# Kernel optimization log

Measured on AMD Instinct MI355X. Metric: run time of the kernel, lower is better.

Reference implementation:

```python
import jax, jax.numpy as jnp
import numpy as np

B, S, H = 4, 1024, 2048      # batch, seq_len, hidden_size
N, D = 16, 128               # num_attention_heads, attention_head_size (num_kv_heads == N)
W_SCALE = 0.02


def setup_inputs() -> dict:
    key = jax.random.key(0)
    ks = jax.random.split(key, 7)
    hidden_states = jax.random.normal(ks[0], (B, S, H), dtype=jnp.float32)
    # Per-head query projections (stacked over the head axis) + shared K/V projections.
    Wq = jax.random.normal(ks[1], (N, H, D), dtype=jnp.float32) * W_SCALE
    bq = jax.random.normal(ks[2], (N, D), dtype=jnp.float32) * W_SCALE
    Wk = jax.random.normal(ks[3], (H, D), dtype=jnp.float32) * W_SCALE
    bk = jax.random.normal(ks[4], (D,), dtype=jnp.float32) * W_SCALE
    Wv = jax.random.normal(ks[5], (H, D), dtype=jnp.float32) * W_SCALE
    bv = jax.random.normal(ks[6], (D,), dtype=jnp.float32) * W_SCALE
    return {"hidden_states": hidden_states, "Wq": Wq, "bq": bq,
            "Wk": Wk, "bk": bk, "Wv": Wv, "bv": bv}


def reference(hidden_states, Wq, bq, Wk, bk, Wv, bv):
    # Batched equivalent of the per-head Python loop:
    # q_i = Linear_i(h); k = key_layer(h); v = value_layer(h) (shared across heads,
    # repeat_interleave is a no-op since num_kv_heads == num_attention_heads).
    Q = jnp.einsum('bsh,nhd->bnsd', hidden_states, Wq) + bq[None, :, None, :]  # [B,N,S,D]
    K = hidden_states @ Wk + bk   # [B,S,D]
    V = hidden_states @ Wv + bv   # [B,S,D]
    # NOTE: source applies no 1/sqrt(D) scaling.
    scores = jnp.einsum('bnsd,btd->bnst', Q, K)          # [B,N,S,S]
    attn = jax.nn.softmax(scores, axis=-1)
    out = jnp.einsum('bnst,btd->bnsd', attn, V)          # [B,N,S,D]
    return out
```

## Files before the change

kernel.cpp:

```cpp
#include <hip/hip_runtime.h>
#include <hip/hip_bf16.h>

typedef unsigned short ushort_t;
typedef _Float16 half_t;
typedef __attribute__((ext_vector_type(8))) _Float16 h8;
typedef __attribute__((ext_vector_type(8))) short short8;
typedef __attribute__((ext_vector_type(4))) short short4_t;
typedef __attribute__((ext_vector_type(4))) float f32x4;
typedef __attribute__((ext_vector_type(4))) float f4;

#define NB 4
#define SS 1024
#define HH 2048
#define NH 16
#define DD 128
#define MM (NB*SS)
#define NTOT 2304
#define COL_K 2048
#define COL_V 2176
#define KVB 64
#define L2E 1.44269504089f

__device__ __forceinline__ ushort_t f2h(float x) {
    half_t h = (half_t)x;
    return *(ushort_t*)&h;
}
__device__ __forceinline__ f32x4 mfma16h(h8 a, h8 b, f32x4 c) {
    return __builtin_amdgcn_mfma_f32_16x16x32_f16(a, b, c, 0, 0, 0);
}
__device__ __forceinline__ void load_lds16(const ushort_t* g, ushort_t* l) {
    __builtin_amdgcn_global_load_lds(
        (const __attribute__((address_space(1))) unsigned int*)g,
        (__attribute__((address_space(3))) unsigned int*)l,
        16, 0, 0);
}

__global__ void k_cvt(const float* __restrict__ src, ushort_t* __restrict__ dst, int n) {
    int i = (blockIdx.x * blockDim.x + threadIdx.x) * 8;
    if (i + 7 < n) {
        f4 a = *(const f4*)(src + i);
        f4 b = *(const f4*)(src + i + 4);
        short8 o;
        #pragma unroll
        for (int j = 0; j < 4; ++j) { o[j] = (short)f2h(a[j]); o[4 + j] = (short)f2h(b[j]); }
        *(short8*)(dst + i) = o;
    }
}

__global__ __launch_bounds__(256) void k_tw(const float* __restrict__ W,
                                            ushort_t* __restrict__ T, int Dd) {
    __shared__ ushort_t t[64][74];
    const int n = blockIdx.z;
    const int h0 = blockIdx.x * 64, d0 = blockIdx.y * 64;
    const int r = threadIdx.x >> 2, cg = (threadIdx.x & 3) * 16;
    const float* src = W + ((size_t)n * HH + h0 + r) * Dd + d0 + cg;
    #pragma unroll
    for (int v = 0; v < 4; ++v) {
        f4 a = *(const f4*)(src + v * 4);
        #pragma unroll
        for (int j = 0; j < 4; ++j) t[r][cg + v * 4 + j] = f2h(a[j]);
    }
    __syncthreads();
    short8 o0, o1;
    #pragma unroll
    for (int j = 0; j < 8; ++j) { o0[j] = (short)t[cg + j][r]; o1[j] = (short)t[cg + 8 + j][r]; }
    ushort_t* dst = T + ((size_t)(n * Dd + d0 + r)) * HH + h0 + cg;
    *(short8*)dst = o0;
    *(short8*)(dst + 8) = o1;
}

__global__ __launch_bounds__(256) void k_gemm(
    const ushort_t* __restrict__ A, const ushort_t* __restrict__ B,
    const float* __restrict__ bq, const float* __restrict__ bk,
    const float* __restrict__ bvv, ushort_t* __restrict__ O,
    ushort_t* __restrict__ Vt) {

    constexpr int BK = 32;
    __shared__ ushort_t sA[128 * BK], sB[128 * BK];

    const int bid = blockIdx.x;
    const int swz = (bid & 7) * 72 + (bid >> 3);
    const int m0 = (swz & 31) * 128;
    const int n0 = (swz >> 5) * 128;

    const int tid = threadIdx.x;
    const int w = tid >> 6, l = tid & 63;
    const int wr = w >> 1, wc = w & 1;
    f32x4 acc[4][4] = {};

    for (int kt = 0; kt < HH / BK; ++kt) {
        const int k0 = kt * BK;
        #pragma unroll
        for (int c = 0; c < 2; ++c) {
            int chunk = c * 4 + w;
            int idx = chunk * 512 + l * 8;
            int row = idx >> 5, kc = idx & 31;
            load_lds16(A + (size_t)(m0 + row) * HH + k0 + kc, &sA[chunk * 512]);
            load_lds16(B + (size_t)(n0 + row) * HH + k0 + kc, &sB[chunk * 512]);
        }
        __syncthreads();

        h8 a[4], b[4];
        #pragma unroll
        for (int i = 0; i < 4; ++i) {
            int ra = wr * 64 + i * 16 + (l & 15);
            int rb = wc * 64 + i * 16 + (l & 15);
            a[i] = *(const h8*)&sA[ra * 32 + (l >> 4) * 8];
            b[i] = *(const h8*)&sB[rb * 32 + (l >> 4) * 8];
        }
        #pragma unroll
        for (int i = 0; i < 4; ++i)
            #pragma unroll
            for (int j = 0; j < 4; ++j)
                acc[i][j] = mfma16h(a[i], b[j], acc[i][j]);
        __syncthreads();
    }

    #pragma unroll
    for (int i = 0; i < 4; ++i) {
        int row = m0 + wr * 64 + i * 16 + ((l >> 4) << 2);
        #pragma unroll
        for (int j = 0; j < 4; ++j) {
            int col = n0 + wc * 64 + j * 16 + (l & 15);
            float bv = (col < COL_K) ? bq[col]
                     : (col < COL_V) ? bk[col - COL_K]
                                     : bvv[col - COL_V];
            if (col < COL_V) {
                #pragma unroll
                for (int r = 0; r < 4; ++r)
                    O[(size_t)(row + r) * NTOT + col] = f2h(acc[i][j][r] + bv);
            } else {
                short4_t o;
                #pragma unroll
                for (int r = 0; r < 4; ++r) o[r] = (short)f2h(acc[i][j][r] + bv);
                *(short4_t*)&Vt[(size_t)(col - COL_V) * MM + row] = o;
            }
        }
    }
}

__global__ __launch_bounds__(512, 4) void k_attn(
    const ushort_t* __restrict__ O, const ushort_t* __restrict__ Vt,
    float* __restrict__ Out) {

    __shared__ ushort_t sK[2][KVB * 128];
    __shared__ ushort_t sVt[2][128 * KVB];

    const int tid = threadIdx.x;
    const int w = tid >> 6, l = tid & 63;
    const int lg = l >> 4, li = l & 15;
    const int q0 = blockIdx.x * 128;
    const int n = blockIdx.y, b = blockIdx.z;

    h8 qv[4];
    {
        size_t base = ((size_t)(b * SS + q0 + w * 16 + li)) * NTOT + n * 128 + lg * 8;
        #pragma unroll
        for (int kk = 0; kk < 4; ++kk)
            qv[kk] = *(const h8*)&O[base + kk * 32];
    }

    f32x4 accO[8] = {};
    float m2 = -3.0e38f;
    float lsum = 0.f;

    auto stage = [&](int bi, int t0) {
        #pragma unroll
        for (int c = 0; c < 2; ++c) {
            int seg = c * 8 + w;
            int oe = seg * 512 + l * 8;
            int row = oe >> 7;
            int mk = (row & 3) | (((row >> 3) & 3) << 2);
            int ce = (oe & 127) ^ (mk << 3);
            size_t g = (size_t)(b * SS + t0 + row) * NTOT + COL_K + ce;
            load_lds16(O + g, &sK[bi][seg * 512]);
        }
        #pragma unroll
        for (int c = 0; c < 2; ++c) {
            int seg = c * 8 + w;
            int oe = seg * 512 + l * 8;
            int row = oe >> 6;
            int ce = (oe & 63) ^ ((row & 7) << 3);
            size_t g = (size_t)row * MM + b * SS + t0 + ce;
            load_lds16(Vt + g, &sVt[bi][seg * 512]);
        }
    };

    stage(0, 0);
    constexpr int NT = SS / KVB;

    for (int it = 0; it < NT; ++it) {
        const int cur = it & 1;
        const int t0 = it * KVB;
        __syncthreads();
        if (it + 1 < NT) stage(cur ^ 1, t0 + KVB);
        const ushort_t* sKc = sK[cur];
        const ushort_t* sVc = sVt[cur];

        f32x4 s[4] = {};
        __builtin_amdgcn_s_setprio(1);
        #pragma unroll
        for (int ts = 0; ts < 4; ++ts) {
            int trow = (ts & 1) * 32 + ((li >> 2) << 3) + ((ts >> 1) << 2) + (li & 3);
            int mk = (trow & 3) | (((trow >> 3) & 3) << 2);
            #pragma unroll
            for (int kk = 0; kk < 4; ++kk) {
                h8 kv = *(const h8*)&sKc[trow * 128 + ((kk * 32 + lg * 8) ^ (mk << 3))];
                s[ts] = mfma16h(kv, qv[kk], s[ts]);
            }
        }
        __builtin_amdgcn_s_setprio(0);

        float v = fmaxf(fmaxf(s[0][0], s[0][1]), fmaxf(s[0][2], s[0][3]));
        #pragma unroll
        for (int ts = 1; ts < 4; ++ts)
            v = fmaxf(v, fmaxf(fmaxf(s[ts][0], s[ts][1]), fmaxf(s[ts][2], s[ts][3])));
        v = fmaxf(v, __shfl_xor(v, 16));
        v = fmaxf(v, __shfl_xor(v, 32));
        float pm2 = v * L2E;

        if (!__all(pm2 <= m2 + 11.54f)) {
            float mn = fmaxf(m2, pm2);
            float scl = exp2f(m2 - mn);
            lsum *= scl;
            #pragma unroll
            for (int db = 0; db < 8; ++db)
                #pragma unroll
                for (int r = 0; r < 4; ++r) accO[db][r] *= scl;
            m2 = mn;
        }

        h8 pb[2];
        #pragma unroll
        for (int ts = 0; ts < 4; ++ts)
            #pragma unroll
            for (int r = 0; r < 4; ++r) {
                float p = exp2f(fmaf(s[ts][r], L2E, -m2));
                lsum += p;
                pb[ts & 1][((ts >> 1) << 2) + r] = (half_t)p;
            }

        __builtin_amdgcn_s_setprio(1);
        #pragma unroll
        for (int db = 0; db < 8; ++db) {
            int d = db * 16 + li;
            const ushort_t* vbase = &sVc[d * KVB];
            int sw = (d & 7) << 3;
            #pragma unroll
            for (int ks = 0; ks < 2; ++ks) {
                h8 va = *(const h8*)&vbase[(ks * 32 + lg * 8) ^ sw];
                accO[db] = mfma16h(va, pb[ks], accO[db]);
            }
        }
        __builtin_amdgcn_s_setprio(0);
    }

    lsum += __shfl_xor(lsum, 16);
    lsum += __shfl_xor(lsum, 32);
    float inv = 1.0f / lsum;
    int q = q0 + w * 16 + li;
    size_t base = (((size_t)b * NH + n) * SS + q) * DD;
    #pragma unroll
    for (int db = 0; db < 8; ++db) {
        f4 o;
        #pragma unroll
        for (int r = 0; r < 4; ++r) o[r] = accO[db][r] * inv;
        *(f4*)&Out[base + db * 16 + lg * 4] = o;
    }
}

#define OFF_HC    ((size_t)0)
#define OFF_BC    (OFF_HC + (size_t)MM*HH*2)
#define OFF_O     (OFF_BC + (size_t)NTOT*HH*2)
#define OFF_VT    (OFF_O + (size_t)MM*NTOT*2)

extern "C" void kernel_launch(void* const* d_in, const int* in_sizes, int n_in,
                              void* d_out, int out_size, void* d_ws, size_t ws_size,
                              hipStream_t stream) {
    const float* hs = (const float*)d_in[0];
    const float* Wq = (const float*)d_in[1];
    const float* bq = (const float*)d_in[2];
    const float* Wk = (const float*)d_in[3];
    const float* bk = (const float*)d_in[4];
    const float* Wv = (const float*)d_in[5];
    const float* bv = (const float*)d_in[6];
    float* out = (float*)d_out;
    char* ws = (char*)d_ws;

    ushort_t* hc   = (ushort_t*)(ws + OFF_HC);
    ushort_t* bcat = (ushort_t*)(ws + OFF_BC);
    ushort_t* Obuf = (ushort_t*)(ws + OFF_O);
    ushort_t* vt   = (ushort_t*)(ws + OFF_VT);

    k_cvt<<<(MM*HH)/(256*8), 256, 0, stream>>>(hs, hc, MM*HH);
    dim3 gwq(HH/64, DD/64, NH);
    k_tw<<<gwq, 256, 0, stream>>>(Wq, bcat, DD);
    dim3 gwk(HH/64, DD/64, 1);
    k_tw<<<gwk, 256, 0, stream>>>(Wk, bcat + (size_t)COL_K*HH, DD);
    k_tw<<<gwk, 256, 0, stream>>>(Wv, bcat + (size_t)COL_V*HH, DD);

    k_gemm<<<(MM/128)*(NTOT/128), 256, 0, stream>>>(hc, bcat, bq, bk, bv, Obuf, vt);

    dim3 ga(SS/128, NH, NB);
    k_attn<<<ga, 512, 0, stream>>>(Obuf, vt, out);
}
```

Baseline: 128.8 us.

## Double-buffer GEMM LDS with BK=64, XOR swizzle, and async prefetch

Restructures the projection GEMM's main loop to double-buffer LDS tiles with a K-step of 64. The next tile is prefetched via direct-to-LDS loads while the current one is consumed, with explicit vmcnt waits and barriers. LDS columns are XOR-swizzled by row to avoid bank conflicts, MFMA issue is wrapped in raised priority, and launch bounds request 2 blocks per CU. The aim is to hide global-load latency and halve barrier count, at the cost of more LDS per block and more dependence on hand-placed waitcnt correctness.

```diff
diff --git a/kernel.cpp b/kernel.cpp
--- a/kernel.cpp
+++ b/kernel.cpp
@@ -69,14 +69,13 @@
     *(short8*)(dst + 8) = o1;
 }
 
-__global__ __launch_bounds__(256) void k_gemm(
+__global__ __launch_bounds__(256, 2) void k_gemm(
     const ushort_t* __restrict__ A, const ushort_t* __restrict__ B,
     const float* __restrict__ bq, const float* __restrict__ bk,
     const float* __restrict__ bvv, ushort_t* __restrict__ O,
     ushort_t* __restrict__ Vt) {
 
-    constexpr int BK = 32;
-    __shared__ ushort_t sA[128 * BK], sB[128 * BK];
+    __shared__ __align__(16) ushort_t lds[2][16384];
 
     const int bid = blockIdx.x;
     const int swz = (bid & 7) * 72 + (bid >> 3);
@@ -85,43 +84,68 @@
 
     const int tid = threadIdx.x;
     const int w = tid >> 6, l = tid & 63;
+    const int lg = l >> 4, li = l & 15;
     const int wr = w >> 1, wc = w & 1;
     f32x4 acc[4][4] = {};
 
-    for (int kt = 0; kt < HH / BK; ++kt) {
-        const int k0 = kt * BK;
-        #pragma unroll
-        for (int c = 0; c < 2; ++c) {
-            int chunk = c * 4 + w;
-            int idx = chunk * 512 + l * 8;
-            int row = idx >> 5, kc = idx & 31;
-            load_lds16(A + (size_t)(m0 + row) * HH + k0 + kc, &sA[chunk * 512]);
-            load_lds16(B + (size_t)(n0 + row) * HH + k0 + kc, &sB[chunk * 512]);
-        }
-        __syncthreads();
-
-        h8 a[4], b[4];
-        #pragma unroll
-        for (int i = 0; i < 4; ++i) {
-            int ra = wr * 64 + i * 16 + (l & 15);
-            int rb = wc * 64 + i * 16 + (l & 15);
-            a[i] = *(const h8*)&sA[ra * 32 + (l >> 4) * 8];
-            b[i] = *(const h8*)&sB[rb * 32 + (l >> 4) * 8];
-        }
-        #pragma unroll
-        for (int i = 0; i < 4; ++i)
-            #pragma unroll
-            for (int j = 0; j < 4; ++j)
-                acc[i][j] = mfma16h(a[i], b[j], acc[i][j]);
-        __syncthreads();
+    auto stage = [&](int buf, int kt) {
+        const int k0 = kt * 64;
+        #pragma unroll
+        for (int c = 0; c < 4; ++c) {
+            int seg = c * 4 + w;
+            int oe = seg * 512 + l * 8;
+            int row = oe >> 6;
+            int ce = (oe & 63) ^ ((row & 7) << 3);
+            load_lds16(A + (size_t)(m0 + row) * HH + k0 + ce, &lds[buf][seg * 512]);
+            load_lds16(B + (size_t)(n0 + row) * HH + k0 + ce, &lds[buf][8192 + seg * 512]);
+        }
+    };
+
+    stage(0, 0);
+    constexpr int NK = HH / 64;
+
+    for (int kt = 0; kt < NK; ++kt) {
+        const int cur = kt & 1;
+        __builtin_amdgcn_s_barrier();
+        if (kt + 1 < NK) {
+            stage(cur ^ 1, kt + 1);
+            asm volatile("s_waitcnt vmcnt(8)" ::: "memory");
+        } else {
+            asm volatile("s_waitcnt vmcnt(0)" ::: "memory");
+        }
+        __builtin_amdgcn_sched_barrier(0);
+        __builtin_amdgcn_s_barrier();
+        __builtin_amdgcn_sched_barrier(0);
+
+        const ushort_t* sA = &lds[cur][0];
+        const ushort_t* sB = &lds[cur][8192];
+        h8 a[2][4], b[2][4];
+        #pragma unroll
+        for (int kk = 0; kk < 2; ++kk)
+            #pragma unroll
+            for (int i = 0; i < 4; ++i) {
+                int ra = wr * 64 + i * 16 + li;
+                int rb = wc * 64 + i * 16 + li;
+                a[kk][i] = *(const h8*)&sA[ra * 64 + ((kk * 32 + lg * 8) ^ ((ra & 7) << 3))];
+                b[kk][i] = *(const h8*)&sB[rb * 64 + ((kk * 32 + lg * 8) ^ ((rb & 7) << 3))];
+            }
+        __builtin_amdgcn_s_setprio(1);
+        #pragma unroll
+        for (int kk = 0; kk < 2; ++kk)
+            #pragma unroll
+            for (int i = 0; i < 4; ++i)
+                #pragma unroll
+                for (int j = 0; j < 4; ++j)
+                    acc[i][j] = mfma16h(a[kk][i], b[kk][j], acc[i][j]);
+        __builtin_amdgcn_s_setprio(0);
     }
 
     #pragma unroll
     for (int i = 0; i < 4; ++i) {
-        int row = m0 + wr * 64 + i * 16 + ((l >> 4) << 2);
+        int row = m0 + wr * 64 + i * 16 + (lg << 2);
         #pragma unroll
         for (int j = 0; j < 4; ++j) {
-            int col = n0 + wc * 64 + j * 16 + (l & 15);
+            int col = n0 + wc * 64 + j * 16 + li;
             float bv = (col < COL_K) ? bq[col]
                      : (col < COL_V) ? bk[col - COL_K]
                                      : bvv[col - COL_V];
```

New measurement: 134.6 us. 4.5% more time.

## Switch attention kernel to 32x32x16 MFMA with 32 query rows per wave

Applied to the files above, without the earlier changes.

Rewrites the attention kernel to use 32x32x16 f16 MFMA instead of 16x16x32, giving each wave 32 query rows and halving the block to 256 threads (4 waves, 128 queries per block). The P matrix is repacked in registers using v_permlane32_swap instead of being reshaped through the old layout. The goal is fewer LDS reads per FLOP and fewer MFMA issues. In exchange each thread holds more accumulator registers, and occupancy drops because of the new launch bounds.

```diff
diff --git a/kernel.cpp b/kernel.cpp
--- a/kernel.cpp
+++ b/kernel.cpp
@@ -7,6 +7,7 @@
 typedef __attribute__((ext_vector_type(8))) short short8;
 typedef __attribute__((ext_vector_type(4))) short short4_t;
 typedef __attribute__((ext_vector_type(4))) float f32x4;
+typedef __attribute__((ext_vector_type(16))) float f32x16;
 typedef __attribute__((ext_vector_type(4))) float f4;
 
 #define NB 4
@@ -27,6 +28,9 @@
 }
 __device__ __forceinline__ f32x4 mfma16h(h8 a, h8 b, f32x4 c) {
     return __builtin_amdgcn_mfma_f32_16x16x32_f16(a, b, c, 0, 0, 0);
+}
+__device__ __forceinline__ f32x16 mfma32h(h8 a, h8 b, f32x16 c) {
+    return __builtin_amdgcn_mfma_f32_32x32x16_f16(a, b, c, 0, 0, 0);
 }
 __device__ __forceinline__ void load_lds16(const ushort_t* g, ushort_t* l) {
     __builtin_amdgcn_global_load_lds(
@@ -139,7 +143,7 @@
     }
 }
 
-__global__ __launch_bounds__(512, 4) void k_attn(
+__global__ __launch_bounds__(256, 2) void k_attn(
     const ushort_t* __restrict__ O, const ushort_t* __restrict__ Vt,
     float* __restrict__ Out) {
 
@@ -148,26 +152,29 @@
 
     const int tid = threadIdx.x;
     const int w = tid >> 6, l = tid & 63;
-    const int lg = l >> 4, li = l & 15;
+    const int li = l & 31, hi = l >> 5;
     const int q0 = blockIdx.x * 128;
     const int n = blockIdx.y, b = blockIdx.z;
-
-    h8 qv[4];
+    const int q = q0 + w * 32 + li;
+
+    const int mkK = (li & 3) | (((li >> 3) & 3) << 2);
+    const int mkV = li & 7;
+
+    h8 qv[8];
     {
-        size_t base = ((size_t)(b * SS + q0 + w * 16 + li)) * NTOT + n * 128 + lg * 8;
-        #pragma unroll
-        for (int kk = 0; kk < 4; ++kk)
-            qv[kk] = *(const h8*)&O[base + kk * 32];
-    }
-
-    f32x4 accO[8] = {};
-    float m2 = -3.0e38f;
-    float lsum = 0.f;
+        size_t base = ((size_t)(b * SS + q)) * NTOT + n * 128 + hi * 8;
+        #pragma unroll
+        for (int c = 0; c < 8; ++c)
+            qv[c] = *(const h8*)&O[base + c * 16];
+    }
+
+    f32x16 acc0 = {}, acc1 = {}, acc2 = {}, acc3 = {};
+    float m2 = -3.0e38f, lsum = 0.f;
 
     auto stage = [&](int bi, int t0) {
         #pragma unroll
-        for (int c = 0; c < 2; ++c) {
-            int seg = c * 8 + w;
+        for (int c = 0; c < 4; ++c) {
+            int seg = c * 4 + w;
             int oe = seg * 512 + l * 8;
             int row = oe >> 7;
             int mk = (row & 3) | (((row >> 3) & 3) << 2);
@@ -176,8 +183,8 @@
             load_lds16(O + g, &sK[bi][seg * 512]);
         }
         #pragma unroll
-        for (int c = 0; c < 2; ++c) {
-            int seg = c * 8 + w;
+        for (int c = 0; c < 4; ++c) {
+            int seg = c * 4 + w;
             int oe = seg * 512 + l * 8;
             int row = oe >> 6;
             int ce = (oe & 63) ^ ((row & 7) << 3);
@@ -191,81 +198,94 @@
 
     for (int it = 0; it < NT; ++it) {
         const int cur = it & 1;
-        const int t0 = it * KVB;
+        const int t0i = it * KVB;
         __syncthreads();
-        if (it + 1 < NT) stage(cur ^ 1, t0 + KVB);
+        if (it + 1 < NT) stage(cur ^ 1, t0i + KVB);
         const ushort_t* sKc = sK[cur];
         const ushort_t* sVc = sVt[cur];
 
-        f32x4 s[4] = {};
+        f32x16 s0 = {}, s1 = {};
         __builtin_amdgcn_s_setprio(1);
         #pragma unroll
-        for (int ts = 0; ts < 4; ++ts) {
-            int trow = (ts & 1) * 32 + ((li >> 2) << 3) + ((ts >> 1) << 2) + (li & 3);
-            int mk = (trow & 3) | (((trow >> 3) & 3) << 2);
-            #pragma unroll
-            for (int kk = 0; kk < 4; ++kk) {
-                h8 kv = *(const h8*)&sKc[trow * 128 + ((kk * 32 + lg * 8) ^ (mk << 3))];
-                s[ts] = mfma16h(kv, qv[kk], s[ts]);
-            }
+        for (int c = 0; c < 8; ++c) {
+            int eo = (c * 16 + hi * 8) ^ (mkK << 3);
+            h8 k0 = *(const h8*)&sKc[li * 128 + eo];
+            h8 k1 = *(const h8*)&sKc[(32 + li) * 128 + eo];
+            s0 = mfma32h(k0, qv[c], s0);
+            s1 = mfma32h(k1, qv[c], s1);
         }
         __builtin_amdgcn_s_setprio(0);
 
-        float v = fmaxf(fmaxf(s[0][0], s[0][1]), fmaxf(s[0][2], s[0][3]));
-        #pragma unroll
-        for (int ts = 1; ts < 4; ++ts)
-            v = fmaxf(v, fmaxf(fmaxf(s[ts][0], s[ts][1]), fmaxf(s[ts][2], s[ts][3])));
-        v = fmaxf(v, __shfl_xor(v, 16));
-        v = fmaxf(v, __shfl_xor(v, 32));
-        float pm2 = v * L2E;
+        float mv = s0[0];
+        #pragma unroll
+        for (int r = 1; r < 16; ++r) mv = fmaxf(mv, s0[r]);
+        #pragma unroll
+        for (int r = 0; r < 16; ++r) mv = fmaxf(mv, s1[r]);
+        mv = fmaxf(mv, __shfl_xor(mv, 32));
+        float pm2 = mv * L2E;
 
         if (!__all(pm2 <= m2 + 11.54f)) {
             float mn = fmaxf(m2, pm2);
             float scl = exp2f(m2 - mn);
             lsum *= scl;
             #pragma unroll
-            for (int db = 0; db < 8; ++db)
-                #pragma unroll
-                for (int r = 0; r < 4; ++r) accO[db][r] *= scl;
+            for (int r = 0; r < 16; ++r) {
+                acc0[r] *= scl; acc1[r] *= scl; acc2[r] *= scl; acc3[r] *= scl;
+            }
             m2 = mn;
         }
 
-        h8 pb[2];
-        #pragma unroll
-        for (int ts = 0; ts < 4; ++ts)
+        unsigned int pk[2][8];
+        #pragma unroll
+        for (int g = 0; g < 2; ++g)
             #pragma unroll
-            for (int r = 0; r < 4; ++r) {
-                float p = exp2f(fmaf(s[ts][r], L2E, -m2));
-                lsum += p;
-                pb[ts & 1][((ts >> 1) << 2) + r] = (half_t)p;
+            for (int j = 0; j < 8; ++j) {
+                float pA = exp2f(fmaf((g ? s1 : s0)[2 * j],     L2E, -m2));
+                float pB = exp2f(fmaf((g ? s1 : s0)[2 * j + 1], L2E, -m2));
+                lsum += pA + pB;
+                union { unsigned int u; half_t h[2]; } pu;
+                pu.h[0] = (half_t)pA; pu.h[1] = (half_t)pB;
+                pk[g][j] = pu.u;
             }
 
         __builtin_amdgcn_s_setprio(1);
         #pragma unroll
-        for (int db = 0; db < 8; ++db) {
-            int d = db * 16 + li;
-            const ushort_t* vbase = &sVc[d * KVB];
-            int sw = (d & 7) << 3;
-            #pragma unroll
-            for (int ks = 0; ks < 2; ++ks) {
-                h8 va = *(const h8*)&vbase[(ks * 32 + lg * 8) ^ sw];
-                accO[db] = mfma16h(va, pb[ks], accO[db]);
-            }
+        for (int tc = 0; tc < 4; ++tc) {
+            const int g = tc >> 1, jb = (tc & 1) * 4;
+            unsigned int a0 = pk[g][jb + 0], b0 = pk[g][jb + 2];
+            unsigned int a1 = pk[g][jb + 1], b1 = pk[g][jb + 3];
+            asm volatile("v_permlane32_swap_b32 %0, %1" : "+v"(a0), "+v"(b0));
+            asm volatile("v_permlane32_swap_b32 %0, %1" : "+v"(a1), "+v"(b1));
+            union { h8 h; unsigned int u[4]; } B2;
+            B2.u[0] = a0; B2.u[1] = a1; B2.u[2] = b0; B2.u[3] = b1;
+
+            int eo = (tc * 16 + hi * 8) ^ (mkV << 3);
+            h8 v0 = *(const h8*)&sVc[(0 * 32 + li) * KVB + eo];
+            h8 v1 = *(const h8*)&sVc[(1 * 32 + li) * KVB + eo];
+            h8 v2 = *(const h8*)&sVc[(2 * 32 + li) * KVB + eo];
+            h8 v3 = *(const h8*)&sVc[(3 * 32 + li) * KVB + eo];
+            acc0 = mfma32h(v0, B2.h, acc0);
+            acc1 = mfma32h(v1, B2.h, acc1);
+            acc2 = mfma32h(v2, B2.h, acc2);
+            acc3 = mfma32h(v3, B2.h, acc3);
         }
         __builtin_amdgcn_s_setprio(0);
     }
 
-    lsum += __shfl_xor(lsum, 16);
     lsum += __shfl_xor(lsum, 32);
     float inv = 1.0f / lsum;
-    int q = q0 + w * 16 + li;
     size_t base = (((size_t)b * NH + n) * SS + q) * DD;
     #pragma unroll
-    for (int db = 0; db < 8; ++db) {
-        f4 o;
-        #pragma unroll
-        for (int r = 0; r < 4; ++r) o[r] = accO[db][r] * inv;
-        *(f4*)&Out[base + db * 16 + lg * 4] = o;
+    for (int dg = 0; dg < 4; ++dg) {
+        const f32x16& ac = (dg == 0) ? acc0 : (dg == 1) ? acc1 : (dg == 2) ? acc2 : acc3;
+        #pragma unroll
+        for (int j = 0; j < 4; ++j) {
+            int d0 = dg * 32 + 8 * j + 4 * hi;
+            f4 o;
+            #pragma unroll
+            for (int r = 0; r < 4; ++r) o[r] = ac[4 * j + r] * inv;
+            *(f4*)&Out[base + d0] = o;
+        }
     }
 }
 
@@ -302,5 +322,5 @@
     k_gemm<<<(MM/128)*(NTOT/128), 256, 0, stream>>>(hc, bcat, bq, bk, bv, Obuf, vt);
 
     dim3 ga(SS/128, NH, NB);
-    k_attn<<<ga, 512, 0, stream>>>(Obuf, vt, out);
-}
+    k_attn<<<ga, 256, 0, stream>>>(Obuf, vt, out);
+}
```

Measured after the change: 133.3 us. 1.04x slower.
